# Optimization experiments

Hardware: AMD Instinct MI355X
Metric: run time of the kernel (lower is better)

The kernel has to match this reference:

```python
import jax, jax.numpy as jnp
import numpy as np

N_NODES = 100000
N_EDGES = 1600000
D_IN = 128
D_HID = 128
D_OUT = 2
N_GRAPHS = 64


def setup_inputs() -> dict:
    key = jax.random.key(0)
    ks = jax.random.split(key, 10)
    x = jax.random.normal(ks[0], (N_NODES, D_IN), dtype=jnp.float32)
    edge_index = jax.random.randint(ks[1], (2, N_EDGES), 0, N_NODES, dtype=jnp.int64)
    batch = jnp.sort(jax.random.randint(ks[2], (N_NODES,), 0, N_GRAPHS, dtype=jnp.int64))
    s_in = 1.0 / np.sqrt(D_IN)
    s_hid = 1.0 / np.sqrt(D_HID)
    W1 = jax.random.uniform(ks[3], (D_IN, D_HID), jnp.float32, -s_in, s_in)
    b1 = jnp.zeros((D_HID,), jnp.float32)
    W2 = jax.random.uniform(ks[4], (D_HID, D_HID), jnp.float32, -s_hid, s_hid)
    b2 = jnp.zeros((D_HID,), jnp.float32)
    W3 = jax.random.uniform(ks[5], (D_HID, D_OUT), jnp.float32, -s_hid, s_hid)
    b3 = jnp.zeros((D_OUT,), jnp.float32)
    return {"x": x, "edge_index": edge_index, "batch": batch,
            "W1": W1, "b1": b1, "W2": W2, "b2": b2, "W3": W3, "b3": b3}


def gcn_conv(x, W, b, src, dst, num_nodes):
    # PyG GCNConv: x' = D^{-1/2} (A + I) D^{-1/2} X W + b, edges flow src -> dst
    h = x @ W  # [N, F] transform first (smaller feature dim path)
    ones = jnp.ones((src.shape[0],), h.dtype)
    deg = jax.ops.segment_sum(ones, dst, num_segments=num_nodes) + 1.0  # self-loop
    dinv = jax.lax.rsqrt(deg)
    norm = dinv[src] * dinv[dst]  # per-edge symmetric normalization
    agg = jax.ops.segment_sum(h[src] * norm[:, None], dst, num_segments=num_nodes)
    out = agg + h * (dinv * dinv)[:, None]  # self-loop contribution
    return out + b


def reference(x, edge_index, batch, W1, b1, W2, b2, W3, b3):
    src, dst = edge_index[0], edge_index[1]
    n = x.shape[0]
    h = jax.nn.relu(gcn_conv(x, W1, b1, src, dst, n))   # dropout is identity in eval
    h = jax.nn.relu(gcn_conv(h, W2, b2, src, dst, n))
    h = gcn_conv(h, W3, b3, src, dst, n)
    # global mean pool over batch segments
    sums = jax.ops.segment_sum(h, batch, num_segments=N_GRAPHS)
    cnts = jax.ops.segment_sum(jnp.ones((n,), h.dtype), batch, num_segments=N_GRAPHS)
    return sums / jnp.maximum(cnts, 1.0)[:, None]
```

## Files before the change

kernel.cpp:

```cpp
#include <hip/hip_runtime.h>
#include <hip/hip_fp16.h>

#define EPB 8192
#define SEGCAP 12288

typedef __attribute__((ext_vector_type(8))) _Float16 half8;
typedef __attribute__((ext_vector_type(4))) float f32x4;
typedef __attribute__((ext_vector_type(4))) int i32x4;


__global__ void scan1(const int* __restrict__ v, int* __restrict__ incl,
                      int* __restrict__ bsum, int n) {
    __shared__ int tmp[256];
    int t = threadIdx.x;
    int gid = blockIdx.x * 256 + t;
    tmp[t] = (gid < n) ? v[gid] : 0;
    __syncthreads();
    for (int off = 1; off < 256; off <<= 1) {
        int x = (t >= off) ? tmp[t - off] : 0;
        __syncthreads();
        tmp[t] += x;
        __syncthreads();
    }
    if (gid < n) incl[gid] = tmp[t];
    if (t == 255) bsum[blockIdx.x] = tmp[255];
}

__global__ void scan2(const int* __restrict__ bsum, int* __restrict__ boff, int nb) {
    __shared__ int tmp[512];
    int t = threadIdx.x;
    int orig = (t < nb) ? bsum[t] : 0;
    tmp[t] = orig;
    __syncthreads();
    for (int off = 1; off < 512; off <<= 1) {
        int x = (t >= off) ? tmp[t - off] : 0;
        __syncthreads();
        tmp[t] += x;
        __syncthreads();
    }
    if (t < nb) boff[t] = tmp[t] - orig;
}

__global__ void basec_k(const int* __restrict__ incl, const int* __restrict__ boff,
                        const int* __restrict__ hist, int* __restrict__ base, int T) {
    int i = blockIdx.x * 256 + threadIdx.x;
    if (i < T) base[i] = incl[i] + boff[blockIdx.x] - hist[i];
}


__global__ __launch_bounds__(256) void hist_k(const int* __restrict__ dst,
                                              int* __restrict__ hist,
                                              int E, int nblk, int nbuk) {
    __shared__ int h[512];
    int t = threadIdx.x;
    for (int i = t; i < nbuk; i += 256) h[i] = 0;
    __syncthreads();
    int start = blockIdx.x * EPB;
    int end = start + EPB; if (end > E) end = E;
    if (end - start == EPB) {
        const i32x4* dv = (const i32x4*)(dst + start);
#pragma unroll
        for (int p = 0; p < 8; ++p) {
            i32x4 d4 = dv[t + p * 256];
            atomicAdd(&h[d4.x >> 8], 1);
            atomicAdd(&h[d4.y >> 8], 1);
            atomicAdd(&h[d4.z >> 8], 1);
            atomicAdd(&h[d4.w >> 8], 1);
        }
    } else {
        for (int e = start + t; e < end; e += 256) atomicAdd(&h[dst[e] >> 8], 1);
    }
    __syncthreads();
    for (int i = t; i < nbuk; i += 256) hist[i * nblk + blockIdx.x] = h[i];
}


__global__ __launch_bounds__(256) void binscatter_k(const int* __restrict__ src,
                                                    const int* __restrict__ dst,
                                                    const int* __restrict__ base,
                                                    unsigned int* __restrict__ binned,
                                                    int E, int nblk, int nbuk) {
    __shared__ int hloc[512];
    __shared__ int lstart[512];
    __shared__ int stmp[512];
    __shared__ unsigned int pk[EPB];
    __shared__ unsigned short bid[EPB];
    int t = threadIdx.x;
    int blk = blockIdx.x;
    int start = blk * EPB;
    int end = start + EPB; if (end > E) end = E;
    int cntE = end - start;

    for (int i = t; i < nbuk; i += 256) hloc[i] = 0;
    __syncthreads();
    for (int e = start + t; e < end; e += 256) atomicAdd(&hloc[dst[e] >> 8], 1);
    __syncthreads();
    for (int i = t; i < 512; i += 256) stmp[i] = (i < nbuk) ? hloc[i] : 0;
    __syncthreads();
    for (int off = 1; off < 512; off <<= 1) {
        int v0 = (t >= off) ? stmp[t - off] : 0;
        int v1 = stmp[t + 256 - off];
        __syncthreads();
        stmp[t] += v0;
        stmp[t + 256] += v1;
        __syncthreads();
    }
    for (int i = t; i < nbuk; i += 256) {
        int ex = stmp[i] - hloc[i];
        lstart[i] = ex;
        hloc[i] = ex;
    }
    __syncthreads();
    for (int e = start + t; e < end; e += 256) {
        int d = dst[e];
        int b = d >> 8;
        int r = atomicAdd(&hloc[b], 1);
        pk[r] = (unsigned int)src[e] | ((unsigned int)(d & 255) << 24);
        bid[r] = (unsigned short)b;
    }
    __syncthreads();
    for (int i = t; i < cntE; i += 256) {
        int b = bid[i];
        binned[base[b * nblk + blk] + (i - lstart[b])] = pk[i];
    }
}


__global__ __launch_bounds__(256) void group_k(const unsigned int* __restrict__ binned,
                                               const int* __restrict__ base,
                                               int* __restrict__ rowptr,
                                               float* __restrict__ dinv,
                                               int* __restrict__ col,
                                               int nblk, int nbuk, int N, int E) {
    __shared__ int cntL[256];
    __shared__ int sc[256];
    __shared__ int cur[256];
    __shared__ int stage[SEGCAP];
    int b = blockIdx.x, t = threadIdx.x;
    int segstart = base[b * nblk];
    int segend = (b + 1 < nbuk) ? base[(b + 1) * nblk] : E;
    int seglen = segend - segstart;

    cntL[t] = 0;
    __syncthreads();
    for (int i = segstart + t; i < segend; i += 256)
        atomicAdd(&cntL[binned[i] >> 24], 1);
    __syncthreads();
    sc[t] = cntL[t];
    __syncthreads();
    for (int off = 1; off < 256; off <<= 1) {
        int v = (t >= off) ? sc[t - off] : 0;
        __syncthreads();
        sc[t] += v;
        __syncthreads();
    }
    int n = (b << 8) + t;
    if (n < N) {
        rowptr[n + 1] = segstart + sc[t];
        dinv[n] = rsqrtf((float)cntL[t] + 1.0f);
    }
    if (b == 0 && t == 0) rowptr[0] = 0;
    cur[t] = sc[t] - cntL[t];
    __syncthreads();
    if (seglen <= SEGCAP) {
        for (int i = segstart + t; i < segend; i += 256) {
            unsigned int p = binned[i];
            int r = atomicAdd(&cur[p >> 24], 1);
            stage[r] = (int)(p & 0xFFFFFFu);
        }
        __syncthreads();
        for (int i = t; i < seglen; i += 256) col[segstart + i] = stage[i];
    } else {
        for (int i = segstart + t; i < segend; i += 256) {
            unsigned int p = binned[i];
            int r = atomicAdd(&cur[p >> 24], 1);
            col[segstart + r] = (int)(p & 0xFFFFFFu);
        }
    }
}


__global__ __launch_bounds__(256) void packW_k(const float* __restrict__ W,
                                               _Float16* __restrict__ Wp) {
    int t = blockIdx.x * 256 + threadIdx.x;
    int lane = t & 63, qct = t >> 6;
    int q = qct >> 3, ct = qct & 7;
    int krow = q * 32 + (lane >> 4) * 8;
    int c = ct * 16 + (lane & 15);
#pragma unroll
    for (int j = 0; j < 8; ++j)
        Wp[(size_t)t * 8 + j] = (_Float16)W[(krow + j) * 128 + c];
}


template<typename XT>
__global__ __launch_bounds__(256) void gemm_mfma(const XT* __restrict__ X,
                                                 const _Float16* __restrict__ Wp,
                                                 const float* __restrict__ dinv,
                                                 _Float16* __restrict__ Gh, int M) {
    constexpr bool F32 = (sizeof(XT) == 4);
    __shared__ _Float16 Wl[16384];
    int t = threadIdx.x;
    for (int i = t; i < 2048; i += 256)
        *(float4*)&Wl[(size_t)i * 8] = ((const float4*)Wp)[i];

    int wid = t >> 6, lane = t & 63;
    int row0 = blockIdx.x * 64 + wid * 16;
    int arow = row0 + (lane & 15); if (arow >= M) arow = M - 1;
    int kgrp = (lane >> 4) * 8;

    half8 a[4];
    if constexpr (F32) {
#pragma unroll
        for (int q = 0; q < 4; ++q) {
            const float* p = (const float*)X + (size_t)arow * 128 + q * 32 + kgrp;
            float4 u = *(const float4*)p;
            float4 v = *(const float4*)(p + 4);
            half8 h;
            h[0] = (_Float16)u.x; h[1] = (_Float16)u.y;
            h[2] = (_Float16)u.z; h[3] = (_Float16)u.w;
            h[4] = (_Float16)v.x; h[5] = (_Float16)v.y;
            h[6] = (_Float16)v.z; h[7] = (_Float16)v.w;
            a[q] = h;
        }
    } else {
#pragma unroll
        for (int q = 0; q < 4; ++q)
            a[q] = *(const half8*)((const _Float16*)X + (size_t)arow * 128 + q * 32 + kgrp);
    }
    __syncthreads();

    f32x4 acc[8];
#pragma unroll
    for (int ct = 0; ct < 8; ++ct) acc[ct] = (f32x4){0.f, 0.f, 0.f, 0.f};

#pragma unroll
    for (int q = 0; q < 4; ++q) {
#pragma unroll
        for (int ct = 0; ct < 8; ++ct) {
            half8 b = *(const half8*)&Wl[(size_t)((q * 8 + ct) * 64 + lane) * 8];
            acc[ct] = __builtin_amdgcn_mfma_f32_16x16x32_f16(a[q], b, acc[ct], 0, 0, 0);
        }
    }

    int rbase = row0 + (lane >> 4) * 4;
#pragma unroll
    for (int reg = 0; reg < 4; ++reg) {
        int r = rbase + reg;
        if (r < M) {
            float di = dinv[r];
#pragma unroll
            for (int ct = 0; ct < 8; ++ct)
                Gh[(size_t)r * 128 + ct * 16 + (lane & 15)] = (_Float16)(acc[ct][reg] * di);
        }
    }
}


__device__ __forceinline__ void addpk(__half2* acc, float4 v) {
    const __half2* h = reinterpret_cast<const __half2*>(&v);
#pragma unroll
    for (int j = 0; j < 4; ++j) acc[j] = __hadd2(acc[j], h[j]);
}

__global__ __launch_bounds__(256) void aggregate128h(const float4* __restrict__ G4,
                                                     const float* __restrict__ dinv,
                                                     const int* __restrict__ rowptr,
                                                     const int* __restrict__ col,
                                                     const float4* __restrict__ bias4,
                                                     float4* __restrict__ OutH, int N) {
    int n = blockIdx.x * 4 + (threadIdx.x >> 6);
    if (n >= N) return;
    int lane = threadIdx.x & 63;
    int f = lane & 15;
    int slot = lane >> 4;
    int e0 = rowptr[n], e1 = rowptr[n + 1];
    __half2 acc[4];
#pragma unroll
    for (int j = 0; j < 4; ++j) acc[j] = __float2half2_rn(0.f);

    int base = e0;
    for (; base + 16 <= e1; base += 16) {
        int s0 = col[base + slot];
        int s1 = col[base + 4 + slot];
        int s2 = col[base + 8 + slot];
        int s3 = col[base + 12 + slot];
        float4 v0 = G4[(size_t)s0 * 16 + f];
        float4 v1 = G4[(size_t)s1 * 16 + f];
        float4 v2 = G4[(size_t)s2 * 16 + f];
        float4 v3 = G4[(size_t)s3 * 16 + f];
        addpk(acc, v0); addpk(acc, v1); addpk(acc, v2); addpk(acc, v3);
    }
    for (int idx = base + slot; idx < e1; idx += 4) {
        float4 v = G4[(size_t)col[idx] * 16 + f];
        addpk(acc, v);
    }
    float a[8];
#pragma unroll
    for (int j = 0; j < 4; ++j) {
        float2 fp = __half22float2(acc[j]);
        a[2 * j] = fp.x;
        a[2 * j + 1] = fp.y;
    }
#pragma unroll
    for (int j = 0; j < 8; ++j) {
        a[j] += __shfl_xor(a[j], 16);
        a[j] += __shfl_xor(a[j], 32);
    }
    if (slot == 0) {
        float4 g = G4[(size_t)n * 16 + f];
        const __half2* sp = (const __half2*)&g;
        float di = dinv[n];
        float4 b0 = bias4[f * 2], b1 = bias4[f * 2 + 1];
        float o[8];
#pragma unroll
        for (int j = 0; j < 4; ++j) {
            float2 fp = __half22float2(sp[j]);
            o[2 * j]     = di * (a[2 * j] + fp.x);
            o[2 * j + 1] = di * (a[2 * j + 1] + fp.y);
        }
        o[0] += b0.x; o[1] += b0.y; o[2] += b0.z; o[3] += b0.w;
        o[4] += b1.x; o[5] += b1.y; o[6] += b1.z; o[7] += b1.w;
#pragma unroll
        for (int j = 0; j < 8; ++j) o[j] = fmaxf(o[j], 0.f);
        __half2 hh[4];
#pragma unroll
        for (int j = 0; j < 4; ++j) hh[j] = __floats2half2_rn(o[2 * j], o[2 * j + 1]);
        OutH[(size_t)n * 16 + f] = *(float4*)hh;
    }
}


__global__ __launch_bounds__(256) void aggregate128h_w3(const float4* __restrict__ G4,
                                                        const float* __restrict__ dinv,
                                                        const int* __restrict__ rowptr,
                                                        const int* __restrict__ col,
                                                        const float4* __restrict__ bias4,
                                                        const float* __restrict__ W3,
                                                        float* __restrict__ G3, int N) {
    int n = blockIdx.x * 4 + (threadIdx.x >> 6);
    if (n >= N) return;
    int lane = threadIdx.x & 63;
    int f = lane & 15;
    int slot = lane >> 4;
    int e0 = rowptr[n], e1 = rowptr[n + 1];
    __half2 acc[4];
#pragma unroll
    for (int j = 0; j < 4; ++j) acc[j] = __float2half2_rn(0.f);

    int base = e0;
    for (; base + 16 <= e1; base += 16) {
        int s0 = col[base + slot];
        int s1 = col[base + 4 + slot];
        int s2 = col[base + 8 + slot];
        int s3 = col[base + 12 + slot];
        float4 v0 = G4[(size_t)s0 * 16 + f];
        float4 v1 = G4[(size_t)s1 * 16 + f];
        float4 v2 = G4[(size_t)s2 * 16 + f];
        float4 v3 = G4[(size_t)s3 * 16 + f];
        addpk(acc, v0); addpk(acc, v1); addpk(acc, v2); addpk(acc, v3);
    }
    for (int idx = base + slot; idx < e1; idx += 4) {
        float4 v = G4[(size_t)col[idx] * 16 + f];
        addpk(acc, v);
    }
    float a[8];
#pragma unroll
    for (int j = 0; j < 4; ++j) {
        float2 fp = __half22float2(acc[j]);
        a[2 * j] = fp.x;
        a[2 * j + 1] = fp.y;
    }
#pragma unroll
    for (int j = 0; j < 8; ++j) {
        a[j] += __shfl_xor(a[j], 16);
        a[j] += __shfl_xor(a[j], 32);
    }
    float p0 = 0.f, p1 = 0.f;
    float di = dinv[n];
    if (slot == 0) {
        float4 g = G4[(size_t)n * 16 + f];
        const __half2* sp = (const __half2*)&g;
        float4 b0 = bias4[f * 2], b1 = bias4[f * 2 + 1];
        float o[8];
#pragma unroll
        for (int j = 0; j < 4; ++j) {
            float2 fp = __half22float2(sp[j]);
            o[2 * j]     = di * (a[2 * j] + fp.x);
            o[2 * j + 1] = di * (a[2 * j + 1] + fp.y);
        }
        o[0] += b0.x; o[1] += b0.y; o[2] += b0.z; o[3] += b0.w;
        o[4] += b1.x; o[5] += b1.y; o[6] += b1.z; o[7] += b1.w;
#pragma unroll
        for (int j = 0; j < 8; ++j) o[j] = fmaxf(o[j], 0.f);
        float w[16];
        *(float4*)&w[0]  = ((const float4*)W3)[f * 4 + 0];
        *(float4*)&w[4]  = ((const float4*)W3)[f * 4 + 1];
        *(float4*)&w[8]  = ((const float4*)W3)[f * 4 + 2];
        *(float4*)&w[12] = ((const float4*)W3)[f * 4 + 3];
#pragma unroll
        for (int j = 0; j < 8; ++j) {
            p0 += o[j] * w[2 * j];
            p1 += o[j] * w[2 * j + 1];
        }
    }
#pragma unroll
    for (int m = 1; m < 16; m <<= 1) {
        p0 += __shfl_xor(p0, m);
        p1 += __shfl_xor(p1, m);
    }
    if (lane == 0) {
        G3[(size_t)n * 2 + 0] = p0 * di;
        G3[(size_t)n * 2 + 1] = p1 * di;
    }
}


__global__ __launch_bounds__(256) void agg2pool(const float2* __restrict__ G3,
                                                const float* __restrict__ dinv,
                                                const int* __restrict__ rowptr,
                                                const int* __restrict__ col,
                                                const float* __restrict__ b3,
                                                const int* __restrict__ batch,
                                                float* __restrict__ pool, int N) {
    __shared__ float ls[192];
    for (int i = threadIdx.x; i < 192; i += 256) ls[i] = 0.f;
    __syncthreads();
    int n = blockIdx.x * 256 + threadIdx.x;
    if (n < N) {
        float s0 = 0.f, s1 = 0.f;
        int e0 = rowptr[n], e1 = rowptr[n + 1];
        int e = e0;
        for (; e + 4 <= e1; e += 4) {
            float2 v0 = G3[col[e]];
            float2 v1 = G3[col[e + 1]];
            float2 v2 = G3[col[e + 2]];
            float2 v3 = G3[col[e + 3]];
            s0 += v0.x + v1.x + v2.x + v3.x;
            s1 += v0.y + v1.y + v2.y + v3.y;
        }
        for (; e < e1; ++e) {
            float2 v = G3[col[e]];
            s0 += v.x; s1 += v.y;
        }
        float2 g = G3[n];
        float di = dinv[n];
        float o0 = di * (s0 + g.x) + b3[0];
        float o1 = di * (s1 + g.y) + b3[1];
        int gb = batch[n];
        atomicAdd(&ls[gb * 3 + 0], o0);
        atomicAdd(&ls[gb * 3 + 1], o1);
        atomicAdd(&ls[gb * 3 + 2], 1.0f);
    }
    __syncthreads();
    for (int i = threadIdx.x; i < 192; i += 256)
        if (ls[i] != 0.f) atomicAdd(&pool[i], ls[i]);
}

__global__ void finalize_k(const float* __restrict__ pool, float* __restrict__ out) {
    int t = threadIdx.x;
    if (t < 128) {
        int g = t >> 1, c = t & 1;
        out[t] = pool[g * 3 + c] / fmaxf(pool[g * 3 + 2], 1.0f);
    }
}


extern "C" void kernel_launch(void* const* d_in, const int* in_sizes, int n_in,
                              void* d_out, int out_size, void* d_ws, size_t ws_size,
                              hipStream_t stream) {
    const float* x   = (const float*)d_in[0];
    const int*  edge = (const int*)d_in[1];
    const int*  batch= (const int*)d_in[2];
    const float* W1  = (const float*)d_in[3];
    const float* b1  = (const float*)d_in[4];
    const float* W2  = (const float*)d_in[5];
    const float* b2  = (const float*)d_in[6];
    const float* W3  = (const float*)d_in[7];
    const float* b3  = (const float*)d_in[8];
    float* out = (float*)d_out;

    int N = in_sizes[0] / 128;
    int E = in_sizes[1] / 2;
    const int* src = edge;
    const int* dst = edge + E;

    int nblk1 = (E + EPB - 1) / EPB;
    int nbuk  = (N + 255) >> 8;
    int T     = nbuk * nblk1;
    int nb2   = (T + 255) / 256;

    char* base_ws = (char*)d_ws;
    size_t off = 0;
    auto alloc = [&](size_t bytes) -> void* {
        void* r = base_ws + off;
        off = (off + bytes + 255) & ~(size_t)255;
        return r;
    };
    _Float16*     GhA    = (_Float16*)alloc((size_t)N * 128 * 2);
    _Float16*     GhB    = (_Float16*)alloc((size_t)N * 128 * 2);
    _Float16*     Wp1    = (_Float16*)alloc(16384 * 2);
    _Float16*     Wp2    = (_Float16*)alloc(16384 * 2);
    float*        dinv   = (float*)alloc((size_t)N * 4);
    int*          rowptr = (int*)alloc((size_t)(N + 1) * 4);
    int*          col    = (int*)alloc((size_t)E * 4);
    unsigned int* binned = (unsigned int*)alloc((size_t)E * 4);
    int*          hist   = (int*)alloc((size_t)T * 4);
    int*          incl   = (int*)alloc((size_t)T * 4);
    int*          bsum   = (int*)alloc(1024 * 4);
    int*          boff   = (int*)alloc(1024 * 4);
    int*          basea  = (int*)alloc((size_t)(T + 1) * 4);
    float*        g3     = (float*)alloc((size_t)N * 2 * 4);
    float*        pool   = (float*)alloc(64 * 3 * 4);

    hipMemsetAsync(pool, 0, 64 * 3 * 4, stream);

    packW_k<<<8, 256, 0, stream>>>(W1, Wp1);
    packW_k<<<8, 256, 0, stream>>>(W2, Wp2);

    hist_k<<<nblk1, 256, 0, stream>>>(dst, hist, E, nblk1, nbuk);
    scan1<<<nb2, 256, 0, stream>>>(hist, incl, bsum, T);
    scan2<<<1, 512, 0, stream>>>(bsum, boff, nb2);
    basec_k<<<nb2, 256, 0, stream>>>(incl, boff, hist, basea, T);
    binscatter_k<<<nblk1, 256, 0, stream>>>(src, dst, basea, binned, E, nblk1, nbuk);
    group_k<<<nbuk, 256, 0, stream>>>(binned, basea, rowptr, dinv, col, nblk1, nbuk, N, E);

    int gb = (N + 63) / 64;
    int ab = (N + 3) / 4;

    gemm_mfma<float><<<gb, 256, 0, stream>>>(x, Wp1, dinv, GhA, N);
    aggregate128h<<<ab, 256, 0, stream>>>((const float4*)GhA, dinv, rowptr, col,
                                          (const float4*)b1, (float4*)GhB, N);
    gemm_mfma<_Float16><<<gb, 256, 0, stream>>>(GhB, Wp2, dinv, GhA, N);
    aggregate128h_w3<<<ab, 256, 0, stream>>>((const float4*)GhA, dinv, rowptr, col,
                                             (const float4*)b2, W3, g3, N);
    agg2pool<<<(N + 255) / 256, 256, 0, stream>>>((const float2*)g3, dinv, rowptr, col,
                                                  b3, batch, pool, N);
    finalize_k<<<1, 128, 0, stream>>>(pool, out);
}
```

Measured before the change: 233.0 us.

## Halve edges per block, merge weight packing, use nontemporal col loads

Several unrelated tweaks land together. Edges per block for the histogram and bin-scatter drop from 8192 to 4096, which doubles block count and needs a larger 1024-thread block-sum scan. The two weight-pack launches are merged into one, and column-index reads in the aggregation kernels become nontemporal so they pollute the cache less and leave more room for the gathered feature rows. Smaller blocks add more histogram partials to scan and write back. Binscatter is assumed to use EPB consistently.

```diff
diff --git a/kernel.cpp b/kernel.cpp
--- a/kernel.cpp
+++ b/kernel.cpp
@@ -1,7 +1,7 @@
 #include <hip/hip_runtime.h>
 #include <hip/hip_fp16.h>
 
-#define EPB 8192
+#define EPB 4096
 #define SEGCAP 12288
 
 typedef __attribute__((ext_vector_type(8))) _Float16 half8;
@@ -27,12 +27,12 @@
 }
 
 __global__ void scan2(const int* __restrict__ bsum, int* __restrict__ boff, int nb) {
-    __shared__ int tmp[512];
+    __shared__ int tmp[1024];
     int t = threadIdx.x;
     int orig = (t < nb) ? bsum[t] : 0;
     tmp[t] = orig;
     __syncthreads();
-    for (int off = 1; off < 512; off <<= 1) {
+    for (int off = 1; off < 1024; off <<= 1) {
         int x = (t >= off) ? tmp[t - off] : 0;
         __syncthreads();
         tmp[t] += x;
@@ -60,7 +60,7 @@
     if (end - start == EPB) {
         const i32x4* dv = (const i32x4*)(dst + start);
 #pragma unroll
-        for (int p = 0; p < 8; ++p) {
+        for (int p = 0; p < EPB / 1024; ++p) {
             i32x4 d4 = dv[t + p * 256];
             atomicAdd(&h[d4.x >> 8], 1);
             atomicAdd(&h[d4.y >> 8], 1);
@@ -180,9 +180,13 @@
 }
 
 
-__global__ __launch_bounds__(256) void packW_k(const float* __restrict__ W,
-                                               _Float16* __restrict__ Wp) {
-    int t = blockIdx.x * 256 + threadIdx.x;
+__global__ __launch_bounds__(256) void packW2_k(const float* __restrict__ W1,
+                                                const float* __restrict__ W2,
+                                                _Float16* __restrict__ Wp1,
+                                                _Float16* __restrict__ Wp2) {
+    const float* W = (blockIdx.x < 8) ? W1 : W2;
+    _Float16* Wp = (blockIdx.x < 8) ? Wp1 : Wp2;
+    int t = (blockIdx.x & 7) * 256 + threadIdx.x;
     int lane = t & 63, qct = t >> 6;
     int q = qct >> 3, ct = qct & 7;
     int krow = q * 32 + (lane >> 4) * 8;
@@ -262,6 +266,7 @@
 #pragma unroll
     for (int j = 0; j < 4; ++j) acc[j] = __hadd2(acc[j], h[j]);
 }
+
 
 __global__ __launch_bounds__(256) void aggregate128h(const float4* __restrict__ G4,
                                                      const float* __restrict__ dinv,
@@ -281,10 +286,10 @@
 
     int base = e0;
     for (; base + 16 <= e1; base += 16) {
-        int s0 = col[base + slot];
-        int s1 = col[base + 4 + slot];
-        int s2 = col[base + 8 + slot];
-        int s3 = col[base + 12 + slot];
+        int s0 = __builtin_nontemporal_load(&col[base + slot]);
+        int s1 = __builtin_nontemporal_load(&col[base + 4 + slot]);
+        int s2 = __builtin_nontemporal_load(&col[base + 8 + slot]);
+        int s3 = __builtin_nontemporal_load(&col[base + 12 + slot]);
         float4 v0 = G4[(size_t)s0 * 16 + f];
         float4 v1 = G4[(size_t)s1 * 16 + f];
         float4 v2 = G4[(size_t)s2 * 16 + f];
@@ -292,7 +297,8 @@
         addpk(acc, v0); addpk(acc, v1); addpk(acc, v2); addpk(acc, v3);
     }
     for (int idx = base + slot; idx < e1; idx += 4) {
-        float4 v = G4[(size_t)col[idx] * 16 + f];
+        int s = __builtin_nontemporal_load(&col[idx]);
+        float4 v = G4[(size_t)s * 16 + f];
         addpk(acc, v);
     }
     float a[8];
@@ -350,10 +356,10 @@
 
     int base = e0;
     for (; base + 16 <= e1; base += 16) {
-        int s0 = col[base + slot];
-        int s1 = col[base + 4 + slot];
-        int s2 = col[base + 8 + slot];
-        int s3 = col[base + 12 + slot];
+        int s0 = __builtin_nontemporal_load(&col[base + slot]);
+        int s1 = __builtin_nontemporal_load(&col[base + 4 + slot]);
+        int s2 = __builtin_nontemporal_load(&col[base + 8 + slot]);
+        int s3 = __builtin_nontemporal_load(&col[base + 12 + slot]);
         float4 v0 = G4[(size_t)s0 * 16 + f];
         float4 v1 = G4[(size_t)s1 * 16 + f];
         float4 v2 = G4[(size_t)s2 * 16 + f];
@@ -361,7 +367,8 @@
         addpk(acc, v0); addpk(acc, v1); addpk(acc, v2); addpk(acc, v3);
     }
     for (int idx = base + slot; idx < e1; idx += 4) {
-        float4 v = G4[(size_t)col[idx] * 16 + f];
+        int s = __builtin_nontemporal_load(&col[idx]);
+        float4 v = G4[(size_t)s * 16 + f];
         addpk(acc, v);
     }
     float a[8];
@@ -432,15 +439,15 @@
         int e0 = rowptr[n], e1 = rowptr[n + 1];
         int e = e0;
         for (; e + 4 <= e1; e += 4) {
-            float2 v0 = G3[col[e]];
-            float2 v1 = G3[col[e + 1]];
-            float2 v2 = G3[col[e + 2]];
-            float2 v3 = G3[col[e + 3]];
+            float2 v0 = G3[__builtin_nontemporal_load(&col[e])];
+            float2 v1 = G3[__builtin_nontemporal_load(&col[e + 1])];
+            float2 v2 = G3[__builtin_nontemporal_load(&col[e + 2])];
+            float2 v3 = G3[__builtin_nontemporal_load(&col[e + 3])];
             s0 += v0.x + v1.x + v2.x + v3.x;
             s1 += v0.y + v1.y + v2.y + v3.y;
         }
         for (; e < e1; ++e) {
-            float2 v = G3[col[e]];
+            float2 v = G3[__builtin_nontemporal_load(&col[e])];
             s0 += v.x; s1 += v.y;
         }
         float2 g = G3[n];
@@ -515,12 +522,11 @@
 
     hipMemsetAsync(pool, 0, 64 * 3 * 4, stream);
 
-    packW_k<<<8, 256, 0, stream>>>(W1, Wp1);
-    packW_k<<<8, 256, 0, stream>>>(W2, Wp2);
+    packW2_k<<<16, 256, 0, stream>>>(W1, W2, Wp1, Wp2);
 
     hist_k<<<nblk1, 256, 0, stream>>>(dst, hist, E, nblk1, nbuk);
     scan1<<<nb2, 256, 0, stream>>>(hist, incl, bsum, T);
-    scan2<<<1, 512, 0, stream>>>(bsum, boff, nb2);
+    scan2<<<1, 1024, 0, stream>>>(bsum, boff, nb2);
     basec_k<<<nb2, 256, 0, stream>>>(incl, boff, hist, basea, T);
     binscatter_k<<<nblk1, 256, 0, stream>>>(src, dst, basea, binned, E, nblk1, nbuk);
     group_k<<<nbuk, 256, 0, stream>>>(binned, basea, rowptr, dinv, col, nblk1, nbuk, N, E);
```

New measurement: 241.6 us. +3.7%, slower.
